# Kernel tuning notes

Measured on AMD Instinct MI355X. Metric: run time of the kernel, lower is better.

Reference implementation:

```python
import jax, jax.numpy as jnp
import numpy as np

B, S, D = 4096, 200, 64
EPS = 1e-3  # keras BatchNormalization default epsilon

def setup_inputs() -> dict:
    key = jax.random.key(0)
    ks = jax.random.split(key, 8)
    return {
        "em": jax.random.normal(ks[0], (B, D), jnp.float32),
        "eu": jax.random.normal(ks[1], (B, D), jnp.float32),
        "Xu": jax.random.normal(ks[2], (B, S, D), jnp.float32),
        "W1": jax.random.normal(ks[3], (4 * D, 64), jnp.float32) * 0.05,
        "b1": jnp.zeros((64,), jnp.float32),
        "W2": jax.random.normal(ks[4], (64, 32), jnp.float32) * 0.1,
        "b2": jnp.zeros((32,), jnp.float32),
        "W3": jax.random.normal(ks[5], (32, 1), jnp.float32) * 0.1,
        "b3": jnp.zeros((1,), jnp.float32),
        "gamma": jnp.ones((2 * D,), jnp.float32),
        "beta": jnp.zeros((2 * D,), jnp.float32),
        "mov_mean": jnp.zeros((2 * D,), jnp.float32),
        "mov_var": jnp.ones((2 * D,), jnp.float32),
    }

def reference(em, eu, Xu, W1, b1, W2, b2, W3, b3, gamma, beta, mov_mean, mov_var):
    # DIN attention: query = em tiled over seq, key = value = Xu
    q = jnp.broadcast_to(em[:, None, :], Xu.shape)            # [B,S,D]
    info = jnp.concatenate([q, Xu, q - Xu, q * Xu], axis=-1)  # [B,S,4D]
    h = jax.nn.relu(info @ W1 + b1)                           # [B,S,64]
    h = jax.nn.relu(h @ W2 + b2)                              # [B,S,32]
    logits = (h @ W3 + b3)[..., 0]                            # [B,S]
    w = jax.nn.softmax(logits, axis=-1)                       # [B,S]
    pooled = jnp.einsum('bs,bsd->bd', w, Xu)                  # [B,D]
    info_all = jnp.concatenate([pooled, em], axis=-1)         # [B,2D]
    bn = (info_all - mov_mean) * jax.lax.rsqrt(mov_var + EPS) * gamma + beta
    return jnp.concatenate([bn, eu], axis=-1)                 # [B,2D+Du]
```

## Files before the change

kernel.cpp:

```cpp
#include <hip/hip_runtime.h>
#include <hip/hip_bf16.h>
#include <math.h>

typedef __bf16 bf16_t;
typedef bf16_t bf16x4 __attribute__((ext_vector_type(4)));
typedef bf16_t bf16x8 __attribute__((ext_vector_type(8)));
typedef float  f32x4  __attribute__((ext_vector_type(4)));

#define SEQ 200
#define SP  208
#define DD  64
#define RS  72

#define MFMA(a, b, c) __builtin_amdgcn_mfma_f32_16x16x32_bf16((a), (b), (c), 0, 0, 0)

__global__ __launch_bounds__(256) void prep_kernel(
    const float* __restrict__ em, const float* __restrict__ W1,
    const float* __restrict__ b1, const float* __restrict__ W2,
    bf16_t* __restrict__ Wbc, bf16_t* __restrict__ W1dt,
    bf16_t* __restrict__ W2t, float* __restrict__ Q)
{
  const int tid = threadIdx.x;
  if (blockIdx.x == 0) {
    for (int i = tid; i < 64 * 64; i += 256) {
      int n = i >> 6, k = i & 63;
      Wbc[i]  = (bf16_t)(W1[(64 + k) * 64 + n] - W1[(128 + k) * 64 + n]);
      W1dt[i] = (bf16_t)(W1[(192 + k) * 64 + n]);
    }
    for (int i = tid; i < 32 * 64; i += 256) {
      int n = i >> 6, k = i & 63;
      W2t[i] = (bf16_t)(W2[k * 32 + n]);
    }
  } else {
    int b = (blockIdx.x - 1) * 4 + (tid >> 6);
    int n = tid & 63;
    float acc = b1[n];
    for (int d = 0; d < 64; ++d)
      acc += em[(size_t)b * 64 + d] * (W1[d * 64 + n] + W1[(128 + d) * 64 + n]);
    Q[(size_t)b * 64 + n] = acc;
  }
}

__global__ __launch_bounds__(256, 4) void din_kernel(
    const float* __restrict__ em, const float* __restrict__ eu,
    const float* __restrict__ Xu, const float* __restrict__ b2,
    const float* __restrict__ W3, const float* __restrict__ b3,
    const float* __restrict__ gam, const float* __restrict__ bet,
    const float* __restrict__ mmean, const float* __restrict__ mvar,
    const bf16_t* __restrict__ Wbc, const bf16_t* __restrict__ W1dt,
    const bf16_t* __restrict__ W2t, const float* __restrict__ Q,
    float* __restrict__ out)
{
  __shared__ __align__(16) bf16_t A[SP * RS];
  __shared__ float logits[SP];
  __shared__ float red[8];
  float* part = (float*)A;

  const int tid  = threadIdx.x;
  const int b    = blockIdx.x;
  const int lane = tid & 63;
  const int wid  = tid >> 6;
  const int g    = lane >> 4;
  const int l16  = lane & 15;
  const int n1   = 16 * wid + l16;

  for (int i = tid; i < 8 * DD; i += 256) {
    int r = SEQ + (i >> 6), c = i & 63;
    A[r * RS + c] = (bf16_t)0.f;
  }

  const float4* Xr = (const float4*)(Xu + (size_t)b * SEQ * DD);
  float4 xg[13];
  #pragma unroll
  for (int k = 0; k < 12; ++k) xg[k] = Xr[tid + 256 * k];
  xg[12] = (tid < 128) ? Xr[tid + 3072] : make_float4(0.f, 0.f, 0.f, 0.f);

  const bf16x8* Wbc8  = (const bf16x8*)Wbc;
  const bf16x8* W1dt8 = (const bf16x8*)W1dt;
  const bf16x8* W2t8  = (const bf16x8*)W2t;
  bf16x8 bB[2];
  #pragma unroll
  for (int c = 0; c < 2; ++c) {
    bf16x8 wbc = Wbc8[n1 * 8 + 4 * c + g];
    bf16x8 w1d = W1dt8[n1 * 8 + 4 * c + g];
    float4 e0 = *(const float4*)&em[(size_t)b * DD + 32 * c + 8 * g];
    float4 e1 = *(const float4*)&em[(size_t)b * DD + 32 * c + 8 * g + 4];
    bB[c][0] = (bf16_t)((float)wbc[0] + e0.x * (float)w1d[0]);
    bB[c][1] = (bf16_t)((float)wbc[1] + e0.y * (float)w1d[1]);
    bB[c][2] = (bf16_t)((float)wbc[2] + e0.z * (float)w1d[2]);
    bB[c][3] = (bf16_t)((float)wbc[3] + e0.w * (float)w1d[3]);
    bB[c][4] = (bf16_t)((float)wbc[4] + e1.x * (float)w1d[4]);
    bB[c][5] = (bf16_t)((float)wbc[5] + e1.y * (float)w1d[5]);
    bB[c][6] = (bf16_t)((float)wbc[6] + e1.z * (float)w1d[6]);
    bB[c][7] = (bf16_t)((float)wbc[7] + e1.w * (float)w1d[7]);
  }
  const float qn   = Q[(size_t)b * DD + n1];
  const float b2v0 = b2[l16], b2v1 = b2[16 + l16];
  const float w3v0 = W3[l16], w3v1 = W3[16 + l16];
  const float b3s  = b3[0];

  bf16x4 xr[13];
  #pragma unroll
  for (int k = 0; k < 13; ++k) {
    bf16x4 xa;
    xa[0] = (bf16_t)xg[k].x; xa[1] = (bf16_t)xg[k].y;
    xa[2] = (bf16_t)xg[k].z; xa[3] = (bf16_t)xg[k].w;
    xr[k] = xa;
    int v = tid + 256 * k;
    if (v < SEQ * DD / 4)
      *(bf16x4*)&A[(v >> 4) * RS + (v & 15) * 4] = xa;
  }
  __syncthreads();

  f32x4 acc[13];
  #pragma unroll
  for (int t = 0; t < 13; ++t) {
    int rb = (16 * t + l16) * RS + 8 * g;
    bf16x8 a0 = *(const bf16x8*)&A[rb];
    bf16x8 a1 = *(const bf16x8*)&A[rb + 32];
    f32x4 a = {0.f, 0.f, 0.f, 0.f};
    a = MFMA(a0, bB[0], a);
    a = MFMA(a1, bB[1], a);
    acc[t] = a;
  }
  __syncthreads();

  #pragma unroll
  for (int t = 0; t < 13; ++t)
    #pragma unroll
    for (int r = 0; r < 4; ++r) {
      float v = acc[t][r] + qn;
      v = v > 0.f ? v : 0.f;
      A[(16 * t + 4 * g + r) * RS + n1] = (bf16_t)v;
    }
  __syncthreads();

  bf16x8 bW2f[2][2];
  #pragma unroll
  for (int c = 0; c < 2; ++c)
    #pragma unroll
    for (int u = 0; u < 2; ++u)
      bW2f[c][u] = W2t8[(16 * u + l16) * 8 + 4 * c + g];

  for (int t = wid; t < 13; t += 4) {
    int rb = (16 * t + l16) * RS + 8 * g;
    bf16x8 h0 = *(const bf16x8*)&A[rb];
    bf16x8 h1 = *(const bf16x8*)&A[rb + 32];
    f32x4 a0 = {0.f, 0.f, 0.f, 0.f}, a1 = {0.f, 0.f, 0.f, 0.f};
    a0 = MFMA(h0, bW2f[0][0], a0);
    a0 = MFMA(h1, bW2f[1][0], a0);
    a1 = MFMA(h0, bW2f[0][1], a1);
    a1 = MFMA(h1, bW2f[1][1], a1);
    #pragma unroll
    for (int r = 0; r < 4; ++r) {
      float p0 = fmaxf(a0[r] + b2v0, 0.f) * w3v0;
      float p1 = fmaxf(a1[r] + b2v1, 0.f) * w3v1;
      float pr = p0 + p1;
      pr += __shfl_xor(pr, 1);
      pr += __shfl_xor(pr, 2);
      pr += __shfl_xor(pr, 4);
      pr += __shfl_xor(pr, 8);
      if (l16 == 0) logits[16 * t + 4 * g + r] = pr + b3s;
    }
  }
  __syncthreads();

  float lv = (tid < SEQ) ? logits[tid] : -INFINITY;
  float mx = lv;
  #pragma unroll
  for (int o = 32; o > 0; o >>= 1) mx = fmaxf(mx, __shfl_xor(mx, o));
  if (lane == 0) red[wid] = mx;
  __syncthreads();
  mx = fmaxf(fmaxf(red[0], red[1]), fmaxf(red[2], red[3]));
  float e = (tid < SEQ) ? __expf(lv - mx) : 0.f;
  if (tid < SEQ) logits[tid] = e;
  float ssum = e;
  #pragma unroll
  for (int o = 32; o > 0; o >>= 1) ssum += __shfl_xor(ssum, o);
  if (lane == 0) red[4 + wid] = ssum;
  __syncthreads();
  const float inv = 1.f / (red[4] + red[5] + red[6] + red[7]);

  {
    float4 ps = {0.f, 0.f, 0.f, 0.f};
    #pragma unroll
    for (int k = 0; k < 13; ++k) {
      int v = tid + 256 * k;
      if (v < SEQ * DD / 4) {
        float w = logits[(tid >> 4) + 16 * k] * inv;
        ps.x += w * (float)xr[k][0];
        ps.y += w * (float)xr[k][1];
        ps.z += w * (float)xr[k][2];
        ps.w += w * (float)xr[k][3];
      }
    }
    *(float4*)&part[(tid >> 4) * 68 + (tid & 15) * 4] = ps;
  }
  __syncthreads();

  if (tid < 192) {
    float v;
    if (tid < 128) {
      float x;
      if (tid < 64) {
        x = 0.f;
        #pragma unroll
        for (int r = 0; r < 16; ++r) x += part[r * 68 + tid];
      } else {
        x = em[(size_t)b * DD + (tid - 64)];
      }
      v = (x - mmean[tid]) * rsqrtf(mvar[tid] + 1e-3f) * gam[tid] + bet[tid];
    } else {
      v = eu[(size_t)b * DD + (tid - 128)];
    }
    out[(size_t)b * 192 + tid] = v;
  }
}

extern "C" void kernel_launch(void* const* d_in, const int* in_sizes, int n_in,
                              void* d_out, int out_size, void* d_ws, size_t ws_size,
                              hipStream_t stream) {
  const float* em = (const float*)d_in[0];
  const float* eu = (const float*)d_in[1];
  const float* Xu = (const float*)d_in[2];
  const float* W1 = (const float*)d_in[3];
  const float* b1 = (const float*)d_in[4];
  const float* W2 = (const float*)d_in[5];
  const float* b2 = (const float*)d_in[6];
  const float* W3 = (const float*)d_in[7];
  const float* b3 = (const float*)d_in[8];
  const float* ga = (const float*)d_in[9];
  const float* be = (const float*)d_in[10];
  const float* mm = (const float*)d_in[11];
  const float* mv = (const float*)d_in[12];
  int B = in_sizes[0] / DD;

  float*  Q    = (float*)d_ws;
  bf16_t* Wbc  = (bf16_t*)((char*)d_ws + (size_t)B * 64 * 4);
  bf16_t* W1dt = Wbc  + 64 * 64;
  bf16_t* W2t  = W1dt + 64 * 64;

  prep_kernel<<<1 + B / 4, 256, 0, stream>>>(em, W1, b1, W2, Wbc, W1dt, W2t, Q);
  din_kernel<<<B, 256, 0, stream>>>(em, eu, Xu, b2, W3, b3, ga, be, mm, mv,
                                    Wbc, W1dt, W2t, Q, (float*)d_out);
}
```

Baseline: 327.3 us.

## Process one batch row per wavefront with streaming online softmax over sequence tiles

Each wavefront now handles one batch row instead of a whole block per row. It streams the 13 sequence tiles from global memory with double-buffered register prefetch and fuses both MLP layers, the logits and an online softmax with pooled accumulation per tile. This removes the block-wide __syncthreads and the large shared staging buffer. The per-row query projection also moves from the prep kernel into the main kernel, so the prep launch shrinks to a single block. In exchange, each wave holds more registers and gets less memory-level parallelism per row, and the occupancy hint drops from 4 to 3.

```diff
diff --git a/kernel.cpp b/kernel.cpp
--- a/kernel.cpp
+++ b/kernel.cpp
@@ -3,218 +3,233 @@
 #include <math.h>
 
 typedef __bf16 bf16_t;
-typedef bf16_t bf16x4 __attribute__((ext_vector_type(4)));
 typedef bf16_t bf16x8 __attribute__((ext_vector_type(8)));
 typedef float  f32x4  __attribute__((ext_vector_type(4)));
 
 #define SEQ 200
-#define SP  208
 #define DD  64
-#define RS  72
+#define RS2 72
 
 #define MFMA(a, b, c) __builtin_amdgcn_mfma_f32_16x16x32_bf16((a), (b), (c), 0, 0, 0)
+#define LGKM0() asm volatile("s_waitcnt lgkmcnt(0)" ::: "memory")
 
 __global__ __launch_bounds__(256) void prep_kernel(
-    const float* __restrict__ em, const float* __restrict__ W1,
-    const float* __restrict__ b1, const float* __restrict__ W2,
+    const float* __restrict__ W1, const float* __restrict__ W2,
     bf16_t* __restrict__ Wbc, bf16_t* __restrict__ W1dt,
-    bf16_t* __restrict__ W2t, float* __restrict__ Q)
+    bf16_t* __restrict__ W2t, float* __restrict__ W1sT)
 {
   const int tid = threadIdx.x;
-  if (blockIdx.x == 0) {
-    for (int i = tid; i < 64 * 64; i += 256) {
-      int n = i >> 6, k = i & 63;
-      Wbc[i]  = (bf16_t)(W1[(64 + k) * 64 + n] - W1[(128 + k) * 64 + n]);
-      W1dt[i] = (bf16_t)(W1[(192 + k) * 64 + n]);
-    }
-    for (int i = tid; i < 32 * 64; i += 256) {
-      int n = i >> 6, k = i & 63;
-      W2t[i] = (bf16_t)(W2[k * 32 + n]);
-    }
-  } else {
-    int b = (blockIdx.x - 1) * 4 + (tid >> 6);
-    int n = tid & 63;
-    float acc = b1[n];
-    for (int d = 0; d < 64; ++d)
-      acc += em[(size_t)b * 64 + d] * (W1[d * 64 + n] + W1[(128 + d) * 64 + n]);
-    Q[(size_t)b * 64 + n] = acc;
+  for (int i = tid; i < 64 * 64; i += 256) {
+    int n = i >> 6, k = i & 63;
+    Wbc[i]  = (bf16_t)(W1[(64 + k) * 64 + n] - W1[(128 + k) * 64 + n]);
+    W1dt[i] = (bf16_t)(W1[(192 + k) * 64 + n]);
+    W1sT[i] = W1[k * 64 + n] + W1[(128 + k) * 64 + n];
+  }
+  for (int i = tid; i < 32 * 64; i += 256) {
+    int n = i >> 6, k = i & 63;
+    W2t[i] = (bf16_t)(W2[k * 32 + n]);
   }
 }
 
-__global__ __launch_bounds__(256, 4) void din_kernel(
+__global__ __launch_bounds__(256, 3) void din_kernel(
     const float* __restrict__ em, const float* __restrict__ eu,
-    const float* __restrict__ Xu, const float* __restrict__ b2,
-    const float* __restrict__ W3, const float* __restrict__ b3,
-    const float* __restrict__ gam, const float* __restrict__ bet,
-    const float* __restrict__ mmean, const float* __restrict__ mvar,
-    const bf16_t* __restrict__ Wbc, const bf16_t* __restrict__ W1dt,
-    const bf16_t* __restrict__ W2t, const float* __restrict__ Q,
-    float* __restrict__ out)
+    const float* __restrict__ Xu, const float* __restrict__ b1,
+    const float* __restrict__ b2, const float* __restrict__ W3,
+    const float* __restrict__ b3, const float* __restrict__ gam,
+    const float* __restrict__ bet, const float* __restrict__ mmean,
+    const float* __restrict__ mvar, const bf16_t* __restrict__ Wbc,
+    const bf16_t* __restrict__ W1dt, const bf16_t* __restrict__ W2t,
+    const float* __restrict__ W1sT, float* __restrict__ out, int Btot)
 {
-  __shared__ __align__(16) bf16_t A[SP * RS];
-  __shared__ float logits[SP];
-  __shared__ float red[8];
-  float* part = (float*)A;
+  __shared__ __align__(16) bf16_t hbuf[4][16 * RS2];
+  __shared__ __align__(16) float  lbuf[4][16];
+  __shared__ __align__(16) float  ebuf[4][64];
 
   const int tid  = threadIdx.x;
-  const int b    = blockIdx.x;
   const int lane = tid & 63;
   const int wid  = tid >> 6;
   const int g    = lane >> 4;
   const int l16  = lane & 15;
-  const int n1   = 16 * wid + l16;
-
-  for (int i = tid; i < 8 * DD; i += 256) {
-    int r = SEQ + (i >> 6), c = i & 63;
-    A[r * RS + c] = (bf16_t)0.f;
-  }
-
-  const float4* Xr = (const float4*)(Xu + (size_t)b * SEQ * DD);
-  float4 xg[13];
-  #pragma unroll
-  for (int k = 0; k < 12; ++k) xg[k] = Xr[tid + 256 * k];
-  xg[12] = (tid < 128) ? Xr[tid + 3072] : make_float4(0.f, 0.f, 0.f, 0.f);
+  const int b    = blockIdx.x * 4 + wid;
+  if (b >= Btot) return;
+
+  bf16_t* hw = hbuf[wid];
+  float*  lw = lbuf[wid];
+  float*  ew = ebuf[wid];
+
+  const float* emr = em + (size_t)b * DD;
+  const float em_l = emr[lane];
+  float4 ef[4];
+  ef[0] = *(const float4*)&emr[8 * g];
+  ef[1] = *(const float4*)&emr[8 * g + 4];
+  ef[2] = *(const float4*)&emr[32 + 8 * g];
+  ef[3] = *(const float4*)&emr[32 + 8 * g + 4];
 
   const bf16x8* Wbc8  = (const bf16x8*)Wbc;
   const bf16x8* W1dt8 = (const bf16x8*)W1dt;
   const bf16x8* W2t8  = (const bf16x8*)W2t;
-  bf16x8 bB[2];
-  #pragma unroll
-  for (int c = 0; c < 2; ++c) {
-    bf16x8 wbc = Wbc8[n1 * 8 + 4 * c + g];
-    bf16x8 w1d = W1dt8[n1 * 8 + 4 * c + g];
-    float4 e0 = *(const float4*)&em[(size_t)b * DD + 32 * c + 8 * g];
-    float4 e1 = *(const float4*)&em[(size_t)b * DD + 32 * c + 8 * g + 4];
-    bB[c][0] = (bf16_t)((float)wbc[0] + e0.x * (float)w1d[0]);
-    bB[c][1] = (bf16_t)((float)wbc[1] + e0.y * (float)w1d[1]);
-    bB[c][2] = (bf16_t)((float)wbc[2] + e0.z * (float)w1d[2]);
-    bB[c][3] = (bf16_t)((float)wbc[3] + e0.w * (float)w1d[3]);
-    bB[c][4] = (bf16_t)((float)wbc[4] + e1.x * (float)w1d[4]);
-    bB[c][5] = (bf16_t)((float)wbc[5] + e1.y * (float)w1d[5]);
-    bB[c][6] = (bf16_t)((float)wbc[6] + e1.z * (float)w1d[6]);
-    bB[c][7] = (bf16_t)((float)wbc[7] + e1.w * (float)w1d[7]);
-  }
-  const float qn   = Q[(size_t)b * DD + n1];
+  bf16x8 bB[4][2];
+  #pragma unroll
+  for (int j = 0; j < 4; ++j)
+    #pragma unroll
+    for (int c = 0; c < 2; ++c) {
+      bf16x8 wbc = Wbc8[(16 * j + l16) * 8 + 4 * c + g];
+      bf16x8 w1d = W1dt8[(16 * j + l16) * 8 + 4 * c + g];
+      float4 e0 = ef[2 * c], e1 = ef[2 * c + 1];
+      bf16x8 r;
+      r[0] = (bf16_t)((float)wbc[0] + e0.x * (float)w1d[0]);
+      r[1] = (bf16_t)((float)wbc[1] + e0.y * (float)w1d[1]);
+      r[2] = (bf16_t)((float)wbc[2] + e0.z * (float)w1d[2]);
+      r[3] = (bf16_t)((float)wbc[3] + e0.w * (float)w1d[3]);
+      r[4] = (bf16_t)((float)wbc[4] + e1.x * (float)w1d[4]);
+      r[5] = (bf16_t)((float)wbc[5] + e1.y * (float)w1d[5]);
+      r[6] = (bf16_t)((float)wbc[6] + e1.z * (float)w1d[6]);
+      r[7] = (bf16_t)((float)wbc[7] + e1.w * (float)w1d[7]);
+      bB[j][c] = r;
+    }
+
+  bf16x8 W2f[2][2];
+  #pragma unroll
+  for (int c = 0; c < 2; ++c)
+    #pragma unroll
+    for (int u = 0; u < 2; ++u)
+      W2f[c][u] = W2t8[(16 * u + l16) * 8 + 4 * c + g];
+
   const float b2v0 = b2[l16], b2v1 = b2[16 + l16];
   const float w3v0 = W3[l16], w3v1 = W3[16 + l16];
   const float b3s  = b3[0];
 
-  bf16x4 xr[13];
-  #pragma unroll
-  for (int k = 0; k < 13; ++k) {
-    bf16x4 xa;
-    xa[0] = (bf16_t)xg[k].x; xa[1] = (bf16_t)xg[k].y;
-    xa[2] = (bf16_t)xg[k].z; xa[3] = (bf16_t)xg[k].w;
-    xr[k] = xa;
-    int v = tid + 256 * k;
-    if (v < SEQ * DD / 4)
-      *(bf16x4*)&A[(v >> 4) * RS + (v & 15) * 4] = xa;
-  }
-  __syncthreads();
-
-  f32x4 acc[13];
+  ew[lane] = em_l;
+  LGKM0();
+  float q = b1[lane];
+  const float4* wq = (const float4*)(W1sT + lane * 64);
+  #pragma unroll
+  for (int dd = 0; dd < 16; ++dd) {
+    float4 wv = wq[dd];
+    float4 ev = *(const float4*)&ew[4 * dd];
+    q += ev.x * wv.x + ev.y * wv.y + ev.z * wv.z + ev.w * wv.w;
+  }
+  float qn[4];
+  #pragma unroll
+  for (int j = 0; j < 4; ++j) qn[j] = __shfl(q, 16 * j + l16);
+
+  float m = -INFINITY, Z = 0.f;
+  float P[16];
+  #pragma unroll
+  for (int e = 0; e < 16; ++e) P[e] = 0.f;
+
+  const float4* Xr = (const float4*)(Xu + (size_t)b * SEQ * DD);
+
+  auto LOADT = [&](int t, float4* X) {
+    if (t == 12 && l16 >= 8) {
+      X[0] = X[1] = X[2] = X[3] = make_float4(0.f, 0.f, 0.f, 0.f);
+    } else {
+      const float4* p = Xr + ((16 * t + l16) * 16 + 2 * g);
+      X[0] = p[0]; X[1] = p[1]; X[2] = p[8]; X[3] = p[9];
+    }
+  };
+
+  auto PROC = [&](int t, const float4* X) {
+    bf16x8 a0, a1;
+    a0[0] = (bf16_t)X[0].x; a0[1] = (bf16_t)X[0].y; a0[2] = (bf16_t)X[0].z; a0[3] = (bf16_t)X[0].w;
+    a0[4] = (bf16_t)X[1].x; a0[5] = (bf16_t)X[1].y; a0[6] = (bf16_t)X[1].z; a0[7] = (bf16_t)X[1].w;
+    a1[0] = (bf16_t)X[2].x; a1[1] = (bf16_t)X[2].y; a1[2] = (bf16_t)X[2].z; a1[3] = (bf16_t)X[2].w;
+    a1[4] = (bf16_t)X[3].x; a1[5] = (bf16_t)X[3].y; a1[6] = (bf16_t)X[3].z; a1[7] = (bf16_t)X[3].w;
+
+    f32x4 c[4];
+    #pragma unroll
+    for (int j = 0; j < 4; ++j) {
+      f32x4 z = {0.f, 0.f, 0.f, 0.f};
+      z = MFMA(a0, bB[j][0], z);
+      z = MFMA(a1, bB[j][1], z);
+      c[j] = z;
+    }
+    #pragma unroll
+    for (int j = 0; j < 4; ++j)
+      #pragma unroll
+      for (int r = 0; r < 4; ++r) {
+        float v = c[j][r] + qn[j];
+        hw[(4 * g + r) * RS2 + 16 * j + l16] = (bf16_t)fmaxf(v, 0.f);
+      }
+    LGKM0();
+    bf16x8 h0 = *(const bf16x8*)&hw[l16 * RS2 + 8 * g];
+    bf16x8 h1 = *(const bf16x8*)&hw[l16 * RS2 + 32 + 8 * g];
+
+    f32x4 d0 = {0.f, 0.f, 0.f, 0.f}, d1 = {0.f, 0.f, 0.f, 0.f};
+    d0 = MFMA(h0, W2f[0][0], d0);
+    d0 = MFMA(h1, W2f[1][0], d0);
+    d1 = MFMA(h0, W2f[0][1], d1);
+    d1 = MFMA(h1, W2f[1][1], d1);
+
+    float pr[4];
+    #pragma unroll
+    for (int r = 0; r < 4; ++r)
+      pr[r] = fmaxf(d0[r] + b2v0, 0.f) * w3v0 + fmaxf(d1[r] + b2v1, 0.f) * w3v1;
+    #pragma unroll
+    for (int o = 1; o < 16; o <<= 1)
+      #pragma unroll
+      for (int r = 0; r < 4; ++r) pr[r] += __shfl_xor(pr[r], o);
+    if (l16 == 0) {
+      #pragma unroll
+      for (int r = 0; r < 4; ++r) {
+        int s = 16 * t + 4 * g + r;
+        lw[4 * g + r] = (s < SEQ) ? (pr[r] + b3s) : -INFINITY;
+      }
+    }
+    LGKM0();
+    float lv = lw[l16];
+
+    float tm = lv;
+    #pragma unroll
+    for (int o = 1; o < 16; o <<= 1) tm = fmaxf(tm, __shfl_xor(tm, o));
+    float mn = fmaxf(m, tm);
+    float al = __expf(m - mn);
+    float ee = __expf(lv - mn);
+    float S = ee;
+    #pragma unroll
+    for (int o = 1; o < 16; o <<= 1) S += __shfl_xor(S, o);
+    Z = Z * al + S;
+    #pragma unroll
+    for (int e = 0; e < 8; ++e) {
+      P[e]     = P[e]     * al + ee * (float)a0[e];
+      P[8 + e] = P[8 + e] * al + ee * (float)a1[e];
+    }
+    m = mn;
+  };
+
+  float4 X0[4], X1[4];
+  LOADT(0, X0);
   #pragma unroll
   for (int t = 0; t < 13; ++t) {
-    int rb = (16 * t + l16) * RS + 8 * g;
-    bf16x8 a0 = *(const bf16x8*)&A[rb];
-    bf16x8 a1 = *(const bf16x8*)&A[rb + 32];
-    f32x4 a = {0.f, 0.f, 0.f, 0.f};
-    a = MFMA(a0, bB[0], a);
-    a = MFMA(a1, bB[1], a);
-    acc[t] = a;
-  }
-  __syncthreads();
-
-  #pragma unroll
-  for (int t = 0; t < 13; ++t)
-    #pragma unroll
-    for (int r = 0; r < 4; ++r) {
-      float v = acc[t][r] + qn;
-      v = v > 0.f ? v : 0.f;
-      A[(16 * t + 4 * g + r) * RS + n1] = (bf16_t)v;
-    }
-  __syncthreads();
-
-  bf16x8 bW2f[2][2];
-  #pragma unroll
-  for (int c = 0; c < 2; ++c)
-    #pragma unroll
-    for (int u = 0; u < 2; ++u)
-      bW2f[c][u] = W2t8[(16 * u + l16) * 8 + 4 * c + g];
-
-  for (int t = wid; t < 13; t += 4) {
-    int rb = (16 * t + l16) * RS + 8 * g;
-    bf16x8 h0 = *(const bf16x8*)&A[rb];
-    bf16x8 h1 = *(const bf16x8*)&A[rb + 32];
-    f32x4 a0 = {0.f, 0.f, 0.f, 0.f}, a1 = {0.f, 0.f, 0.f, 0.f};
-    a0 = MFMA(h0, bW2f[0][0], a0);
-    a0 = MFMA(h1, bW2f[1][0], a0);
-    a1 = MFMA(h0, bW2f[0][1], a1);
-    a1 = MFMA(h1, bW2f[1][1], a1);
-    #pragma unroll
-    for (int r = 0; r < 4; ++r) {
-      float p0 = fmaxf(a0[r] + b2v0, 0.f) * w3v0;
-      float p1 = fmaxf(a1[r] + b2v1, 0.f) * w3v1;
-      float pr = p0 + p1;
-      pr += __shfl_xor(pr, 1);
-      pr += __shfl_xor(pr, 2);
-      pr += __shfl_xor(pr, 4);
-      pr += __shfl_xor(pr, 8);
-      if (l16 == 0) logits[16 * t + 4 * g + r] = pr + b3s;
-    }
-  }
-  __syncthreads();
-
-  float lv = (tid < SEQ) ? logits[tid] : -INFINITY;
-  float mx = lv;
-  #pragma unroll
-  for (int o = 32; o > 0; o >>= 1) mx = fmaxf(mx, __shfl_xor(mx, o));
-  if (lane == 0) red[wid] = mx;
-  __syncthreads();
-  mx = fmaxf(fmaxf(red[0], red[1]), fmaxf(red[2], red[3]));
-  float e = (tid < SEQ) ? __expf(lv - mx) : 0.f;
-  if (tid < SEQ) logits[tid] = e;
-  float ssum = e;
-  #pragma unroll
-  for (int o = 32; o > 0; o >>= 1) ssum += __shfl_xor(ssum, o);
-  if (lane == 0) red[4 + wid] = ssum;
-  __syncthreads();
-  const float inv = 1.f / (red[4] + red[5] + red[6] + red[7]);
-
-  {
-    float4 ps = {0.f, 0.f, 0.f, 0.f};
-    #pragma unroll
-    for (int k = 0; k < 13; ++k) {
-      int v = tid + 256 * k;
-      if (v < SEQ * DD / 4) {
-        float w = logits[(tid >> 4) + 16 * k] * inv;
-        ps.x += w * (float)xr[k][0];
-        ps.y += w * (float)xr[k][1];
-        ps.z += w * (float)xr[k][2];
-        ps.w += w * (float)xr[k][3];
-      }
-    }
-    *(float4*)&part[(tid >> 4) * 68 + (tid & 15) * 4] = ps;
-  }
-  __syncthreads();
-
-  if (tid < 192) {
-    float v;
-    if (tid < 128) {
-      float x;
-      if (tid < 64) {
-        x = 0.f;
-        #pragma unroll
-        for (int r = 0; r < 16; ++r) x += part[r * 68 + tid];
-      } else {
-        x = em[(size_t)b * DD + (tid - 64)];
-      }
-      v = (x - mmean[tid]) * rsqrtf(mvar[tid] + 1e-3f) * gam[tid] + bet[tid];
-    } else {
-      v = eu[(size_t)b * DD + (tid - 128)];
-    }
-    out[(size_t)b * 192 + tid] = v;
-  }
+    float4* cur = (t & 1) ? X1 : X0;
+    float4* nxt = (t & 1) ? X0 : X1;
+    if (t < 12) LOADT(t + 1, nxt);
+    PROC(t, cur);
+  }
+
+  const float invZ = 1.f / Z;
+  #pragma unroll
+  for (int o = 1; o < 16; o <<= 1)
+    #pragma unroll
+    for (int e = 0; e < 16; ++e) P[e] += __shfl_xor(P[e], o);
+  float* pw = (float*)hw;
+  if (l16 == 0) {
+    #pragma unroll
+    for (int e = 0; e < 8; ++e) {
+      pw[8 * g + e]      = P[e]     * invZ;
+      pw[32 + 8 * g + e] = P[8 + e] * invZ;
+    }
+  }
+  LGKM0();
+  float pooled = pw[lane];
+
+  float o0 = (pooled - mmean[lane]) * rsqrtf(mvar[lane] + 1e-3f) * gam[lane] + bet[lane];
+  float o1 = (em_l - mmean[64 + lane]) * rsqrtf(mvar[64 + lane] + 1e-3f) * gam[64 + lane] + bet[64 + lane];
+  float o2 = eu[(size_t)b * 64 + lane];
+  float* ob = out + (size_t)b * 192;
+  ob[lane]       = o0;
+  ob[64 + lane]  = o1;
+  ob[128 + lane] = o2;
 }
 
 extern "C" void kernel_launch(void* const* d_in, const int* in_sizes, int n_in,
@@ -235,12 +250,13 @@
   const float* mv = (const float*)d_in[12];
   int B = in_sizes[0] / DD;
 
-  float*  Q    = (float*)d_ws;
-  bf16_t* Wbc  = (bf16_t*)((char*)d_ws + (size_t)B * 64 * 4);
-  bf16_t* W1dt = Wbc  + 64 * 64;
+  float*  W1sT = (float*)d_ws;
+  bf16_t* Wbc  = (bf16_t*)((char*)d_ws + 64 * 64 * 4);
+  bf16_t* W1dt = Wbc + 64 * 64;
   bf16_t* W2t  = W1dt + 64 * 64;
 
-  prep_kernel<<<1 + B / 4, 256, 0, stream>>>(em, W1, b1, W2, Wbc, W1dt, W2t, Q);
-  din_kernel<<<B, 256, 0, stream>>>(em, eu, Xu, b2, W3, b3, ga, be, mm, mv,
-                                    Wbc, W1dt, W2t, Q, (float*)d_out);
+  prep_kernel<<<1, 256, 0, stream>>>(W1, W2, Wbc, W1dt, W2t, W1sT);
+  din_kernel<<<(B + 3) / 4, 256, 0, stream>>>(em, eu, Xu, b1, b2, W3, b3, ga, be,
+                                              mm, mv, Wbc, W1dt, W2t, W1sT,
+                                              (float*)d_out, B);
 }
```

After: 401.3 us. 1.23x slower.
